# Optimization experiments

Hardware: AMD Instinct MI355X
Metric: run time of the kernel (lower is better)

## Reference

```python
import jax, jax.numpy as jnp
import numpy as np

B, SEQ, D, H, L, DFF, K = 2, 2048, 256, 8, 2, 1024, 3
DK = D // H
EPS = 1e-5
DROP_CONNECT = 0.5  # eval mode: weight * (1 - rate)


def _make_pe():
    pos = np.arange(SEQ)[:, None].astype(np.float32)
    div = np.exp(np.arange(0, D, 2).astype(np.float32) * (-np.log(10000.0) / D))
    pe = np.zeros((SEQ, D), np.float32)
    pe[:, 0::2] = np.sin(pos * div)
    pe[:, 1::2] = np.cos(pos * div)
    return jnp.asarray(pe)


def setup_inputs() -> dict:
    key = jax.random.key(0)
    ks = jax.random.split(key, 16)
    s = 0.02
    d = {
        'x': jax.random.normal(ks[0], (B, SEQ, 1), jnp.float32),
        'conv_w': jax.random.normal(ks[1], (D, 1, K), jnp.float32) * s,
        'conv_b': jnp.zeros((D,), jnp.float32),
        'bn_g': jnp.ones((D,), jnp.float32),
        'bn_b': jnp.zeros((D,), jnp.float32),
        'pe': _make_pe(),
        'qW': jax.random.normal(ks[2], (L, D, D), jnp.float32) * s,
        'qb': jnp.zeros((L, D), jnp.float32),
        'kW': jax.random.normal(ks[3], (L, D, D), jnp.float32) * s,
        'kb': jnp.zeros((L, D), jnp.float32),
        'vW': jax.random.normal(ks[4], (L, D, D), jnp.float32) * s,
        'vb': jnp.zeros((L, D), jnp.float32),
        'oW': jax.random.normal(ks[5], (L, D, D), jnp.float32) * s,
        'ob': jnp.zeros((L, D), jnp.float32),
        'scale': jnp.ones((L,), jnp.float32),
        'td': jnp.ones((L, H), jnp.float32),
        'ln1g': jnp.ones((L, D), jnp.float32),
        'ln1b': jnp.zeros((L, D), jnp.float32),
        'f1W': jax.random.normal(ks[6], (L, DFF, D), jnp.float32) * s,
        'f1b': jnp.zeros((L, DFF), jnp.float32),
        'f2W': jax.random.normal(ks[7], (L, D, DFF), jnp.float32) * s,
        'f2b': jnp.zeros((L, D), jnp.float32),
        'ln2g': jnp.ones((L, D), jnp.float32),
        'ln2b': jnp.zeros((L, D), jnp.float32),
        'outW': jax.random.normal(ks[8], (1, D), jnp.float32) * s,
        'outb': jnp.zeros((1,), jnp.float32),
    }
    return d


def _layernorm(z, g, b):
    m = z.mean(-1, keepdims=True)
    v = ((z - m) ** 2).mean(-1, keepdims=True)
    return (z - m) / jnp.sqrt(v + EPS) * g + b


def reference(x, conv_w, conv_b, bn_g, bn_b, pe, qW, qb, kW, kb, vW, vb, oW, ob,
              scale, td, ln1g, ln1b, f1W, f1b, f2W, f2b, ln2g, ln2b, outW, outb):
    # CNN frontend: [B,S,1] -> [B,1,S] -> conv -> BN(eval) -> relu -> [B,S,D]
    h = jnp.transpose(x, (0, 2, 1))
    h = jax.lax.conv_general_dilated(h, conv_w, (1,), 'SAME',
                                     dimension_numbers=('NCH', 'OIH', 'NCH'))
    h = h + conv_b[None, :, None]
    # BatchNorm eval with running_mean=0, running_var=1
    h = h / jnp.sqrt(1.0 + EPS) * bn_g[None, :, None] + bn_b[None, :, None]
    h = jax.nn.relu(h)
    h = jnp.transpose(h, (0, 2, 1)) + pe[None]

    inv_sqrt_dk = 1.0 / np.sqrt(DK).astype(np.float32)
    key_pos = jnp.arange(SEQ, dtype=h.dtype)  # decay depends on key index only

    for l in range(L):
        q = (h @ qW[l].T + qb[l]).reshape(B, SEQ, H, DK).transpose(0, 2, 1, 3)
        k = (h @ kW[l].T + kb[l]).reshape(B, SEQ, H, DK).transpose(0, 2, 1, 3)
        v = (h @ vW[l].T + vb[l]).reshape(B, SEQ, H, DK).transpose(0, 2, 1, 3)
        scores = jnp.einsum('bhqd,bhkd->bhqk', q, k) * (inv_sqrt_dk * scale[l])
        decay = jnp.exp(-td[l][:, None, None] * key_pos[None, None, :])  # [H,1,S]
        scores = scores * decay[None]
        attn = jax.nn.softmax(scores, axis=-1) * jax.nn.sigmoid(scores)
        ctx = jnp.einsum('bhqk,bhkd->bhqd', attn, v)
        ctx = ctx.transpose(0, 2, 1, 3).reshape(B, SEQ, D)
        h = _layernorm(h + (ctx @ oW[l].T + ob[l]), ln1g[l], ln1b[l])
        ff = jax.nn.relu(h @ f1W[l].T + f1b[l]) @ f2W[l].T + f2b[l]
        h = _layernorm(h + ff, ln2g[l], ln2b[l])

    last = h[:, -1, :]
    # DropConnectLinear in eval: weight * (1 - drop_connect_rate)
    return last @ (outW * (1.0 - DROP_CONNECT)).T + outb
```

## Files before the change

kernel.cpp:

```cpp
#include <hip/hip_runtime.h>
#include <math.h>

#define B_    2
#define SEQ_  2048
#define D_    256
#define H_    8
#define DK_   32
#define L_    2
#define DFF_  1024

#define TD_CUT 44.0f

typedef short  bf16x8 __attribute__((ext_vector_type(8)));
typedef float  f32x4  __attribute__((ext_vector_type(4)));

__device__ __forceinline__ int compute_kcut(float tdv) {
    int kcut = SEQ_;
    if (tdv > 1e-9f) {
        float kc = TD_CUT / tdv;
        kcut = (kc >= (float)SEQ_) ? SEQ_ : ((int)kc + 1);
    }
    int kcr = (kcut + 31) & ~31;
    if (kcr > SEQ_) kcr = SEQ_;
    return kcr;
}

__device__ __forceinline__ unsigned short f2bf(float f) {
    unsigned int u = __float_as_uint(f);
    unsigned int r = u + 0x7FFFu + ((u >> 16) & 1u);
    return (unsigned short)(r >> 16);
}
__device__ __forceinline__ float bf2f(unsigned short u) {
    return __uint_as_float(((unsigned int)u) << 16);
}

__device__ __forceinline__ void gload_lds16(const unsigned short* g, unsigned short* l) {
    __builtin_amdgcn_global_load_lds(
        (const __attribute__((address_space(1))) unsigned int*)(const unsigned int*)g,
        (__attribute__((address_space(3))) unsigned int*)(unsigned int*)l,
        16, 0, 0);
}

__global__ __launch_bounds__(256) void prep_kernel(
    const float* __restrict__ x, const float* __restrict__ w,
    const float* __restrict__ cb, const float* __restrict__ bg,
    const float* __restrict__ bb, const float* __restrict__ pe,
    float* __restrict__ h, unsigned short* __restrict__ hbf,
    const float* __restrict__ p0, const float* __restrict__ p1,
    const float* __restrict__ p2, const float* __restrict__ p3,
    const float* __restrict__ p4, const float* __restrict__ p5,
    unsigned short* __restrict__ q0, unsigned short* __restrict__ q1,
    unsigned short* __restrict__ q2, unsigned short* __restrict__ q3,
    unsigned short* __restrict__ q4, unsigned short* __restrict__ q5,
    float* __restrict__ vtail)
{
    int bid = blockIdx.x;
    if (bid < 4) vtail[bid * 256 + threadIdx.x] = 0.f;
    if (bid < 768) {
        int t = bid * 256 + threadIdx.x;
        const float* src; unsigned short* dst; int base;
        if (t < 65536) {
            int a = t >> 14;
            src = a == 0 ? p0 : a == 1 ? p1 : a == 2 ? p2 : p3;
            dst = a == 0 ? q0 : a == 1 ? q1 : a == 2 ? q2 : q3;
            base = (t & 16383) * 8;
        } else {
            int u = t - 65536;
            int a = u >> 16;
            src = a ? p5 : p4;
            dst = a ? q5 : q4;
            base = (u & 65535) * 8;
        }
        float4 v0 = *(const float4*)(src + base);
        float4 v1 = *(const float4*)(src + base + 4);
        bf16x8 o;
        o[0] = (short)f2bf(v0.x); o[1] = (short)f2bf(v0.y);
        o[2] = (short)f2bf(v0.z); o[3] = (short)f2bf(v0.w);
        o[4] = (short)f2bf(v1.x); o[5] = (short)f2bf(v1.y);
        o[6] = (short)f2bf(v1.z); o[7] = (short)f2bf(v1.w);
        *(bf16x8*)(dst + base) = o;
        return;
    }
    int idx = (bid - 768) * 256 + threadIdx.x;
    int d = idx & 255;
    int s = (idx >> 8) & 2047;
    int b = idx >> 19;

    const float* xp = x + b * SEQ_;
    float xm1 = (s > 0)        ? xp[s - 1] : 0.f;
    float x0  = xp[s];
    float xp1 = (s < SEQ_ - 1) ? xp[s + 1] : 0.f;

    float acc = xm1 * w[d * 3 + 0] + x0 * w[d * 3 + 1] + xp1 * w[d * 3 + 2];
    acc += cb[d];
    acc = acc * rsqrtf(1.f + 1e-5f) * bg[d] + bb[d];
    acc = fmaxf(acc, 0.f);
    float v = acc + pe[s * D_ + d];
    h[idx] = v;
    hbf[idx] = f2bf(v);
}

__global__ __launch_bounds__(256) void gemm_qkv(
    const unsigned short* __restrict__ A,
    const unsigned short* __restrict__ W0, const unsigned short* __restrict__ W1,
    const unsigned short* __restrict__ W2,
    const float* __restrict__ b0, const float* __restrict__ b1,
    const float* __restrict__ b2,
    unsigned short* __restrict__ O0, unsigned short* __restrict__ O1,
    unsigned short* __restrict__ O2,
    const float* __restrict__ td_l, float* __restrict__ vtail_l,
    int M, int N, int K)
{
    int z = blockIdx.z;
    const unsigned short* W = (z == 0) ? W0 : (z == 1) ? W1 : W2;
    const float* bias = (z == 0) ? b0 : (z == 1) ? b1 : b2;
    unsigned short* C = (z == 0) ? O0 : (z == 1) ? O1 : O2;

    __shared__ unsigned short As[64 * 32];
    __shared__ unsigned short Bs[64 * 32];
    __shared__ float vsc[4][2][16];

    int tid  = threadIdx.x;
    int wave = tid >> 6, lane = tid & 63;
    int wm = (wave & 1) * 32, wn = (wave >> 1) * 32;
    int bm = blockIdx.y * 64, bn = blockIdx.x * 64;

    int sr  = tid >> 2;
    int scb = (tid & 3) ^ ((sr >> 1) & 3);
    const unsigned short* aG = A + (size_t)(bm + sr) * K + scb * 8;
    const unsigned short* wG = W + (size_t)(bn + sr) * K + scb * 8;
    unsigned short* aL = &As[tid * 8];
    unsigned short* bL = &Bs[tid * 8];

    int fr = lane & 15;
    int kb = lane >> 4;
    int cb = (kb ^ ((fr >> 1) & 3)) * 8;
    int oA0 = (wm + fr) * 32 + cb;
    int oA1 = (wm + 16 + fr) * 32 + cb;
    int oB0 = (wn + fr) * 32 + cb;
    int oB1 = (wn + 16 + fr) * 32 + cb;

    f32x4 acc[2][2];
#pragma unroll
    for (int i = 0; i < 2; ++i)
#pragma unroll
        for (int j = 0; j < 2; ++j) acc[i][j] = (f32x4){0.f, 0.f, 0.f, 0.f};

    for (int k0 = 0; k0 < K; k0 += 32) {
        __syncthreads();
        gload_lds16(aG + k0, aL);
        gload_lds16(wG + k0, bL);
        __syncthreads();

        bf16x8 a0f = *(const bf16x8*)&As[oA0];
        bf16x8 a1f = *(const bf16x8*)&As[oA1];
        bf16x8 b0f = *(const bf16x8*)&Bs[oB0];
        bf16x8 b1f = *(const bf16x8*)&Bs[oB1];

        acc[0][0] = __builtin_amdgcn_mfma_f32_16x16x32_bf16(a0f, b0f, acc[0][0], 0, 0, 0);
        acc[0][1] = __builtin_amdgcn_mfma_f32_16x16x32_bf16(a0f, b1f, acc[0][1], 0, 0, 0);
        acc[1][0] = __builtin_amdgcn_mfma_f32_16x16x32_bf16(a1f, b0f, acc[1][0], 0, 0, 0);
        acc[1][1] = __builtin_amdgcn_mfma_f32_16x16x32_bf16(a1f, b1f, acc[1][1], 0, 0, 0);
    }

    int crow = (lane >> 4) * 4;
    int ccol = lane & 15;
    float psum[2] = {0.f, 0.f};
    int kc[2];
    kc[0] = compute_kcut(td_l[(bn + wn) >> 5]);
    kc[1] = compute_kcut(td_l[(bn + wn + 16) >> 5]);

#pragma unroll
    for (int j = 0; j < 2; ++j) {
        float bj = bias[bn + wn + j * 16 + ccol];
#pragma unroll
        for (int i = 0; i < 2; ++i) {
#pragma unroll
            for (int r = 0; r < 4; ++r) {
                float v = acc[i][j][r] + bj;
                unsigned short ubf = f2bf(v);
                C[(size_t)(bm + wm + i * 16 + crow + r) * N + bn + wn + j * 16 + ccol] = ubf;
                if (z == 2) {
                    int srow = (bm + wm + i * 16 + crow + r) & 2047;
                    if (srow >= kc[j]) psum[j] += bf2f(ubf);
                }
            }
        }
    }

    if (z == 2) {
#pragma unroll
        for (int j = 0; j < 2; ++j) {
            psum[j] += __shfl_xor(psum[j], 16);
            psum[j] += __shfl_xor(psum[j], 32);
        }
        if (lane < 16) { vsc[wave][0][lane] = psum[0]; vsc[wave][1][lane] = psum[1]; }
        __syncthreads();
        if (tid < 64) {
            int wh = tid >> 5, jj = (tid >> 4) & 1, cc = tid & 15;
            float s = vsc[2 * wh][jj][cc] + vsc[2 * wh + 1][jj][cc];
            int b = blockIdx.y >> 5;
            atomicAdd(&vtail_l[b * 256 + bn + wh * 32 + jj * 16 + cc], s);
        }
    }
}

__global__ __launch_bounds__(128) void attn_kernel(
    const unsigned short* __restrict__ q, const unsigned short* __restrict__ k,
    const unsigned short* __restrict__ v, const float* __restrict__ vtail_l,
    unsigned short* __restrict__ ctxbf,
    const float* __restrict__ scale_p, const float* __restrict__ td_l)
{
    int b = blockIdx.z, hh = blockIdx.y;
    int tid = threadIdx.x;
    int row = tid >> 2;
    int sp  = tid & 3;
    int qrow = blockIdx.x * 32 + row;

    float sc  = 0.17677669529663687f * scale_p[0];
    float tdv = td_l[hh];
    int kcr = compute_kcut(tdv);
    int ntiles = kcr >> 5;

    __shared__ float kt[32][36];
    __shared__ float vt[32][36];
    __shared__ float Os[4][32][36];
    __shared__ float ms[4][32], ls[4][32];
    __shared__ float vts[32];

    if (tid < 32) vts[tid] = vtail_l[b * 256 + hh * 32 + tid];

    const unsigned short* qptr = q + ((size_t)(b * SEQ_ + qrow)) * D_ + hh * DK_;
    float qreg[32];
#pragma unroll
    for (int j = 0; j < 4; ++j) {
        uint4 u = ((const uint4*)qptr)[j];
        qreg[j*8+0] = __uint_as_float(u.x << 16); qreg[j*8+1] = __uint_as_float(u.x & 0xFFFF0000u);
        qreg[j*8+2] = __uint_as_float(u.y << 16); qreg[j*8+3] = __uint_as_float(u.y & 0xFFFF0000u);
        qreg[j*8+4] = __uint_as_float(u.z << 16); qreg[j*8+5] = __uint_as_float(u.z & 0xFFFF0000u);
        qreg[j*8+6] = __uint_as_float(u.w << 16); qreg[j*8+7] = __uint_as_float(u.w & 0xFFFF0000u);
    }
    float O[32];
#pragma unroll
    for (int d = 0; d < 32; ++d) O[d] = 0.f;
    float mrun = -1e30f, lrun = 0.f;

    for (int t = 0; t < ntiles; ++t) {
        int k0 = t * 32;
        __syncthreads();
        {
            int r = tid >> 2, c8 = (tid & 3) * 8;
            size_t goff = ((size_t)(b * SEQ_ + k0 + r)) * D_ + hh * DK_ + c8;
            uint4 uk = *(const uint4*)(k + goff);
            uint4 uv = *(const uint4*)(v + goff);
            *(float4*)&kt[r][c8]     = make_float4(__uint_as_float(uk.x << 16), __uint_as_float(uk.x & 0xFFFF0000u),
                                                   __uint_as_float(uk.y << 16), __uint_as_float(uk.y & 0xFFFF0000u));
            *(float4*)&kt[r][c8 + 4] = make_float4(__uint_as_float(uk.z << 16), __uint_as_float(uk.z & 0xFFFF0000u),
                                                   __uint_as_float(uk.w << 16), __uint_as_float(uk.w & 0xFFFF0000u));
            *(float4*)&vt[r][c8]     = make_float4(__uint_as_float(uv.x << 16), __uint_as_float(uv.x & 0xFFFF0000u),
                                                   __uint_as_float(uv.y << 16), __uint_as_float(uv.y & 0xFFFF0000u));
            *(float4*)&vt[r][c8 + 4] = make_float4(__uint_as_float(uv.z << 16), __uint_as_float(uv.z & 0xFFFF0000u),
                                                   __uint_as_float(uv.w << 16), __uint_as_float(uv.w & 0xFFFF0000u));
        }
        __syncthreads();

        float sb[8];
        float tmax = -1e30f;
#pragma unroll
        for (int kk = 0; kk < 8; ++kk) {
            int kl = sp * 8 + kk;
            float acc = 0.f;
#pragma unroll
            for (int d4 = 0; d4 < 8; ++d4) {
                float4 kv = *(const float4*)&kt[kl][d4 * 4];
                acc += qreg[d4 * 4 + 0] * kv.x + qreg[d4 * 4 + 1] * kv.y
                     + qreg[d4 * 4 + 2] * kv.z + qreg[d4 * 4 + 3] * kv.w;
            }
            float dec = __expf(-tdv * (float)(k0 + kl));
            float sv = acc * sc * dec;
            sb[kk] = sv;
            tmax = fmaxf(tmax, sv);
        }
        float mnew = fmaxf(mrun, tmax);
        float alpha = __expf(mrun - mnew);
        lrun *= alpha;
#pragma unroll
        for (int d = 0; d < 32; ++d) O[d] *= alpha;
#pragma unroll
        for (int kk = 0; kk < 8; ++kk) {
            int kl = sp * 8 + kk;
            float sv = sb[kk];
            float e = __expf(sv - mnew);
            float sg = 1.f / (1.f + __expf(-sv));
            float p = e * sg;
            lrun += e;
#pragma unroll
            for (int d4 = 0; d4 < 8; ++d4) {
                float4 vv = *(const float4*)&vt[kl][d4 * 4];
                O[d4 * 4 + 0] += p * vv.x; O[d4 * 4 + 1] += p * vv.y;
                O[d4 * 4 + 2] += p * vv.z; O[d4 * 4 + 3] += p * vv.w;
            }
        }
        mrun = mnew;
    }

#pragma unroll
    for (int d4 = 0; d4 < 8; ++d4)
        *(float4*)&Os[sp][row][d4 * 4] =
            make_float4(O[d4*4+0], O[d4*4+1], O[d4*4+2], O[d4*4+3]);
    ms[sp][row] = mrun;
    ls[sp][row] = lrun;
    __syncthreads();

    {
        int g = sp;
        float m0 = fmaxf(fmaxf(ms[0][row], ms[1][row]), fmaxf(ms[2][row], ms[3][row]));
        float mt = (kcr < SEQ_) ? fmaxf(m0, 0.f) : m0;
        float w0 = __expf(ms[0][row] - mt), w1 = __expf(ms[1][row] - mt);
        float w2 = __expf(ms[2][row] - mt), w3 = __expf(ms[3][row] - mt);
        float Lt = ls[0][row]*w0 + ls[1][row]*w1 + ls[2][row]*w2 + ls[3][row]*w3;
        float ew = 0.f;
        if (kcr < SEQ_) {
            ew = __expf(-mt);
            Lt += (float)(SEQ_ - kcr) * ew;
        }
        float invL = 1.f / Lt;
        unsigned int packed[4];
#pragma unroll
        for (int dd = 0; dd < 8; dd += 2) {
            int d0 = g * 8 + dd, d1 = d0 + 1;
            float n0 = Os[0][row][d0]*w0 + Os[1][row][d0]*w1 + Os[2][row][d0]*w2 + Os[3][row][d0]*w3;
            float n1 = Os[0][row][d1]*w0 + Os[1][row][d1]*w1 + Os[2][row][d1]*w2 + Os[3][row][d1]*w3;
            if (kcr < SEQ_) {
                n0 += 0.5f * ew * vts[d0];
                n1 += 0.5f * ew * vts[d1];
            }
            packed[dd >> 1] = (unsigned)f2bf(n0 * invL) | ((unsigned)f2bf(n1 * invL) << 16);
        }
        unsigned short* obf = ctxbf + ((size_t)(b * SEQ_ + qrow)) * D_ + hh * DK_ + g * 8;
        *(uint4*)obf = make_uint4(packed[0], packed[1], packed[2], packed[3]);
    }
}

__global__ __launch_bounds__(256) void oproj_ln1(
    const unsigned short* __restrict__ ctx, const unsigned short* __restrict__ wo,
    const float* __restrict__ ob, const float* __restrict__ resid,
    const float* __restrict__ g1, const float* __restrict__ bt1,
    float* __restrict__ h1out, unsigned short* __restrict__ h1bf)
{
    __shared__ unsigned short As[16 * 32];
    __shared__ unsigned short Bs[256 * 32];
    __shared__ float lsum[4][16], lsq[4][16], mean_s[16], inv_s[16];

    int tid = threadIdx.x;
    int wave = tid >> 6, lane = tid & 63;
    int bm = blockIdx.x * 16;
    int fr = lane & 15, kb = lane >> 4;
    int q = kb, cl = fr;
    int swz = (fr >> 1) & 3;

    const unsigned short* gpB[4];
    unsigned short* lpB[4];
#pragma unroll
    for (int i = 0; i < 4; ++i) {
        int sB = i * 256 + tid;
        int r = sB >> 2, ck = (sB & 3) ^ ((r >> 1) & 3);
        gpB[i] = wo + (size_t)r * 256 + ck * 8;
        lpB[i] = &Bs[sB * 8];
    }
    const unsigned short* gpA = nullptr;
    unsigned short* lpA = nullptr;
    if (tid < 64) {
        int r = tid >> 2, ck = (tid & 3) ^ ((r >> 1) & 3);
        gpA = ctx + (size_t)(bm + r) * 256 + ck * 8;
        lpA = &As[tid * 8];
    }

    int oA = fr * 32 + ((kb ^ swz) * 8);
    int oB[4];
#pragma unroll
    for (int t = 0; t < 4; ++t) {
        int n = wave * 64 + t * 16 + fr;
        oB[t] = n * 32 + ((kb ^ swz) * 8);
    }

    f32x4 acc[4];
#pragma unroll
    for (int j = 0; j < 4; ++j) acc[j] = (f32x4){0.f, 0.f, 0.f, 0.f};

    for (int k0 = 0; k0 < 256; k0 += 32) {
        __syncthreads();
#pragma unroll
        for (int i = 0; i < 4; ++i) gload_lds16(gpB[i] + k0, lpB[i]);
        if (tid < 64) gload_lds16(gpA + k0, lpA);
        __syncthreads();

        bf16x8 af = *(const bf16x8*)&As[oA];
#pragma unroll
        for (int j = 0; j < 4; ++j)
            acc[j] = __builtin_amdgcn_mfma_f32_16x16x32_bf16(
                af, *(const bf16x8*)&Bs[oB[j]], acc[j], 0, 0, 0);
    }

    float zsum[4] = {0.f, 0.f, 0.f, 0.f}, zsq[4] = {0.f, 0.f, 0.f, 0.f};
    float zv[4][4];
#pragma unroll
    for (int ct = 0; ct < 4; ++ct) {
        int col = wave * 64 + ct * 16 + cl;
        float bj = ob[col];
#pragma unroll
        for (int r = 0; r < 4; ++r) {
            int row = bm + q * 4 + r;
            float z = acc[ct][r] + bj + resid[(size_t)row * 256 + col];
            zv[ct][r] = z;
            zsum[r] += z;
            zsq[r]  += z * z;
        }
    }
#pragma unroll
    for (int r = 0; r < 4; ++r) {
#pragma unroll
        for (int off = 1; off < 16; off <<= 1) {
            zsum[r] += __shfl_xor(zsum[r], off);
            zsq[r]  += __shfl_xor(zsq[r], off);
        }
    }
    if (cl == 0) {
#pragma unroll
        for (int r = 0; r < 4; ++r) {
            lsum[wave][q * 4 + r] = zsum[r];
            lsq[wave][q * 4 + r]  = zsq[r];
        }
    }
    __syncthreads();
    if (tid < 16) {
        float s  = lsum[0][tid] + lsum[1][tid] + lsum[2][tid] + lsum[3][tid];
        float sq = lsq[0][tid] + lsq[1][tid] + lsq[2][tid] + lsq[3][tid];
        float mean = s * (1.f / 256.f);
        float var  = sq * (1.f / 256.f) - mean * mean;
        mean_s[tid] = mean;
        inv_s[tid]  = rsqrtf(var + 1e-5f);
    }
    __syncthreads();

#pragma unroll
    for (int ct = 0; ct < 4; ++ct) {
        int col = wave * 64 + ct * 16 + cl;
        float gc = g1[col], bc = bt1[col];
#pragma unroll
        for (int r = 0; r < 4; ++r) {
            int lr = q * 4 + r;
            float o = (zv[ct][r] - mean_s[lr]) * inv_s[lr] * gc + bc;
            size_t off = (size_t)(bm + lr) * 256 + col;
            h1out[off] = o;
            h1bf[off]  = f2bf(o);
        }
    }
}

__global__ __launch_bounds__(256) void ffn_fused(
    const unsigned short* __restrict__ h1bf, const unsigned short* __restrict__ w1,
    const float* __restrict__ f1b, const unsigned short* __restrict__ w2,
    float* __restrict__ part)
{
    __shared__ unsigned short As[32 * 32];
    __shared__ unsigned short Bs[256 * 32];
    __shared__ unsigned short ffs[32 * 264];

    int tid = threadIdx.x;
    int wave = tid >> 6, lane = tid & 63;
    int c = blockIdx.x;
    int bm = blockIdx.y * 32;
    int fr = lane & 15, kb = lane >> 4;
    int q = kb, cl = fr;
    int swz = (fr >> 1) & 3;

    const unsigned short* gA = nullptr;
    unsigned short* lA = nullptr;
    if (tid < 128) {
        int ar = tid >> 2, ack = (tid & 3) ^ ((ar >> 1) & 3);
        gA = h1bf + (size_t)(bm + ar) * 256 + ack * 8;
        lA = &As[tid * 8];
    }

    int oA1[2], oB[4];
#pragma unroll
    for (int t = 0; t < 2; ++t) {
        int m = t * 16 + fr;
        oA1[t] = m * 32 + ((kb ^ ((m >> 1) & 3)) * 8);
    }
#pragma unroll
    for (int t = 0; t < 4; ++t) {
        int n = wave * 64 + t * 16 + fr;
        oB[t] = n * 32 + ((kb ^ ((n >> 1) & 3)) * 8);
    }

    f32x4 a1[2][4];
#pragma unroll
    for (int i = 0; i < 2; ++i)
#pragma unroll
        for (int j = 0; j < 4; ++j) a1[i][j] = (f32x4){0.f, 0.f, 0.f, 0.f};

    for (int ks = 0; ks < 8; ++ks) {
        __syncthreads();
        if (tid < 128) gload_lds16(gA + ks * 32, lA);
#pragma unroll
        for (int i = 0; i < 4; ++i) {
            int sB = i * 256 + tid;
            int r = sB >> 2, ck = (sB & 3) ^ ((r >> 1) & 3);
            gload_lds16(w1 + (size_t)(c * 256 + r) * 256 + ks * 32 + ck * 8, &Bs[sB * 8]);
        }
        __syncthreads();

        bf16x8 af[2], bfv[4];
#pragma unroll
        for (int t = 0; t < 2; ++t) af[t] = *(const bf16x8*)&As[oA1[t]];
#pragma unroll
        for (int t = 0; t < 4; ++t) bfv[t] = *(const bf16x8*)&Bs[oB[t]];
#pragma unroll
        for (int i = 0; i < 2; ++i)
#pragma unroll
            for (int j = 0; j < 4; ++j)
                a1[i][j] = __builtin_amdgcn_mfma_f32_16x16x32_bf16(af[i], bfv[j], a1[i][j], 0, 0, 0);
    }

#pragma unroll
    for (int ct = 0; ct < 4; ++ct) {
        int col = wave * 64 + ct * 16 + cl;
        float bj = f1b[c * 256 + col];
#pragma unroll
        for (int rt = 0; rt < 2; ++rt)
#pragma unroll
            for (int r = 0; r < 4; ++r) {
                float v = fmaxf(a1[rt][ct][r] + bj, 0.f);
                ffs[(rt * 16 + q * 4 + r) * 264 + col] = f2bf(v);
            }
    }

    f32x4 a2[2][4];
#pragma unroll
    for (int i = 0; i < 2; ++i)
#pragma unroll
        for (int j = 0; j < 4; ++j) a2[i][j] = (f32x4){0.f, 0.f, 0.f, 0.f};

    for (int ks = 0; ks < 8; ++ks) {
        __syncthreads();
#pragma unroll
        for (int i = 0; i < 4; ++i) {
            int sB = i * 256 + tid;
            int r = sB >> 2, ck = (sB & 3) ^ ((r >> 1) & 3);
            gload_lds16(w2 + (size_t)r * 1024 + c * 256 + ks * 32 + ck * 8, &Bs[sB * 8]);
        }
        __syncthreads();

        bf16x8 af[2], bfv[4];
#pragma unroll
        for (int t = 0; t < 2; ++t)
            af[t] = *(const bf16x8*)&ffs[(t * 16 + fr) * 264 + ks * 32 + kb * 8];
#pragma unroll
        for (int t = 0; t < 4; ++t) bfv[t] = *(const bf16x8*)&Bs[oB[t]];
#pragma unroll
        for (int i = 0; i < 2; ++i)
#pragma unroll
            for (int j = 0; j < 4; ++j)
                a2[i][j] = __builtin_amdgcn_mfma_f32_16x16x32_bf16(af[i], bfv[j], a2[i][j], 0, 0, 0);
    }

#pragma unroll
    for (int ct = 0; ct < 4; ++ct) {
        int col = wave * 64 + ct * 16 + cl;
#pragma unroll
        for (int rt = 0; rt < 2; ++rt)
#pragma unroll
            for (int r = 0; r < 4; ++r)
                part[((size_t)c * 4096 + bm + rt * 16 + q * 4 + r) * 256 + col] = a2[rt][ct][r];
    }
}

__global__ __launch_bounds__(256) void merge_ln2(
    const float* __restrict__ h1, const float* __restrict__ part,
    const float* __restrict__ f2b, const float* __restrict__ g2,
    const float* __restrict__ bt2,
    float* __restrict__ hout, unsigned short* __restrict__ hbf,
    const float* __restrict__ outW, const float* __restrict__ outb,
    float* __restrict__ out, int doFinal)
{
    int row = blockIdx.x * 4 + (threadIdx.x >> 6);
    int lane = threadIdx.x & 63;
    int d = lane * 4;

    float4 z = *(const float4*)(h1 + (size_t)row * 256 + d);
    float4 b4 = *(const float4*)(f2b + d);
    z.x += b4.x; z.y += b4.y; z.z += b4.z; z.w += b4.w;
#pragma unroll
    for (int c = 0; c < 4; ++c) {
        float4 p = *(const float4*)(part + ((size_t)c * 4096 + row) * 256 + d);
        z.x += p.x; z.y += p.y; z.z += p.z; z.w += p.w;
    }

    float s = z.x + z.y + z.z + z.w;
    float ss = z.x * z.x + z.y * z.y + z.z * z.z + z.w * z.w;
#pragma unroll
    for (int off = 1; off < 64; off <<= 1) {
        s += __shfl_xor(s, off);
        ss += __shfl_xor(ss, off);
    }
    float mean = s * (1.f / 256.f);
    float var = ss * (1.f / 256.f) - mean * mean;
    float inv = rsqrtf(var + 1e-5f);

    float4 g4 = *(const float4*)(g2 + d);
    float4 t4 = *(const float4*)(bt2 + d);
    float4 o;
    o.x = (z.x - mean) * inv * g4.x + t4.x;
    o.y = (z.y - mean) * inv * g4.y + t4.y;
    o.z = (z.z - mean) * inv * g4.z + t4.z;
    o.w = (z.w - mean) * inv * g4.w + t4.w;
    *(float4*)(hout + (size_t)row * 256 + d) = o;
    unsigned int u01 = (unsigned)f2bf(o.x) | ((unsigned)f2bf(o.y) << 16);
    unsigned int u23 = (unsigned)f2bf(o.z) | ((unsigned)f2bf(o.w) << 16);
    *(uint2*)&hbf[(size_t)row * 256 + d] = make_uint2(u01, u23);

    if (doFinal && (row == 2047 || row == 4095)) {
        float4 w4 = *(const float4*)(outW + d);
        float s2 = o.x * w4.x + o.y * w4.y + o.z * w4.z + o.w * w4.w;
#pragma unroll
        for (int off = 1; off < 64; off <<= 1) s2 += __shfl_xor(s2, off);
        if (lane == 0) out[row >> 11] = s2 * 0.5f + outb[0];
    }
}

extern "C" void kernel_launch(void* const* d_in, const int* in_sizes, int n_in,
                              void* d_out, int out_size, void* d_ws, size_t ws_size,
                              hipStream_t stream)
{
    (void)in_sizes; (void)n_in; (void)out_size; (void)ws_size;
    const float* x      = (const float*)d_in[0];
    const float* conv_w = (const float*)d_in[1];
    const float* conv_b = (const float*)d_in[2];
    const float* bn_g   = (const float*)d_in[3];
    const float* bn_b   = (const float*)d_in[4];
    const float* pe     = (const float*)d_in[5];
    const float* qW     = (const float*)d_in[6];
    const float* qb     = (const float*)d_in[7];
    const float* kW     = (const float*)d_in[8];
    const float* kb     = (const float*)d_in[9];
    const float* vW     = (const float*)d_in[10];
    const float* vb     = (const float*)d_in[11];
    const float* oW     = (const float*)d_in[12];
    const float* ob     = (const float*)d_in[13];
    const float* scale  = (const float*)d_in[14];
    const float* td     = (const float*)d_in[15];
    const float* ln1g   = (const float*)d_in[16];
    const float* ln1b   = (const float*)d_in[17];
    const float* f1W    = (const float*)d_in[18];
    const float* f1b    = (const float*)d_in[19];
    const float* f2W    = (const float*)d_in[20];
    const float* f2b    = (const float*)d_in[21];
    const float* ln2g   = (const float*)d_in[22];
    const float* ln2b   = (const float*)d_in[23];
    const float* outW   = (const float*)d_in[24];
    const float* outb   = (const float*)d_in[25];
    float* out = (float*)d_out;

    float* ws = (float*)d_ws;
    const size_t MT = (size_t)B_ * SEQ_ * D_;
    float* h     = ws;
    float* h1    = ws + MT;
    float* part  = ws + 2 * MT;
    float* vtail = ws + 6 * MT;
    unsigned short* bfb = (unsigned short*)(ws + 6 * MT + 1024);
    unsigned short* h_bf   = bfb;
    unsigned short* ctx_bf = bfb + MT;
    unsigned short* q_bf   = bfb + 2 * MT;
    unsigned short* k_bf   = bfb + 3 * MT;
    unsigned short* v_bf   = bfb + 4 * MT;
    unsigned short* h1_bf  = bfb + 5 * MT;
    unsigned short* wq_bf  = bfb + 6 * MT;
    unsigned short* wk_bf  = wq_bf + MT / 8;
    unsigned short* wv_bf  = wk_bf + MT / 8;
    unsigned short* wo_bf  = wv_bf + MT / 8;
    unsigned short* wf1_bf = wo_bf + MT / 8;
    unsigned short* wf2_bf = wf1_bf + MT / 2;

    const int Mrows = B_ * SEQ_;

    prep_kernel<<<768 + (B_ * SEQ_ * D_) / 256, 256, 0, stream>>>(
        x, conv_w, conv_b, bn_g, bn_b, pe, h, h_bf,
        qW, kW, vW, oW, f1W, f2W,
        wq_bf, wk_bf, wv_bf, wo_bf, wf1_bf, wf2_bf, vtail);

    for (int l = 0; l < L_; ++l) {
        const unsigned short* wq_l  = wq_bf  + (size_t)l * D_ * D_;
        const unsigned short* wk_l  = wk_bf  + (size_t)l * D_ * D_;
        const unsigned short* wv_l  = wv_bf  + (size_t)l * D_ * D_;
        const unsigned short* wo_l  = wo_bf  + (size_t)l * D_ * D_;
        const unsigned short* wf1_l = wf1_bf + (size_t)l * DFF_ * D_;
        const unsigned short* wf2_l = wf2_bf + (size_t)l * DFF_ * D_;
        float* vtail_l = vtail + l * B_ * 256;

        gemm_qkv<<<dim3(D_ / 64, Mrows / 64, 3), 256, 0, stream>>>(
            h_bf, wq_l, wk_l, wv_l, qb + l * D_, kb + l * D_, vb + l * D_,
            q_bf, k_bf, v_bf, td + l * H_, vtail_l, Mrows, D_, D_);

        attn_kernel<<<dim3(SEQ_ / 32, H_, B_), 128, 0, stream>>>(
            q_bf, k_bf, v_bf, vtail_l, ctx_bf, scale + l, td + l * H_);

        oproj_ln1<<<Mrows / 16, 256, 0, stream>>>(
            ctx_bf, wo_l, ob + l * D_, h,
            ln1g + l * D_, ln1b + l * D_, h1, h1_bf);

        ffn_fused<<<dim3(4, Mrows / 32), 256, 0, stream>>>(
            h1_bf, wf1_l, f1b + l * DFF_, wf2_l, part);

        merge_ln2<<<Mrows / 4, 256, 0, stream>>>(
            h1, part, f2b + l * D_, ln2g + l * D_, ln2b + l * D_,
            h, h_bf, outW, outb, out, (l == L_ - 1) ? 1 : 0);
    }
}
```

Before: 204.9 us.

## Double GEMM K-tile to 64 with XOR swizzle and halve oproj row tile

Widens the K tile from 32 to 64 in the QKV, o-proj and FFN GEMMs and switches to an 8-way XOR swizzle, so each main loop needs half as many barrier pairs and the MFMAs see twice the work per sync. The o-proj+LN1 kernel now handles 8 rows per block instead of 16, with zero padding in LDS for the unused MFMA rows, which doubles the grid for more parallelism. In exchange, LDS use per block grows (the o-proj B tile goes from 16 KB to 32 KB, and FFN uses more too), which may lower occupancy. Half of the o-proj MFMA rows are now wasted work, and the wo weights are reloaded by twice as many blocks.

```diff
diff --git a/kernel.cpp b/kernel.cpp
--- a/kernel.cpp
+++ b/kernel.cpp
@@ -116,8 +116,8 @@
     const float* bias = (z == 0) ? b0 : (z == 1) ? b1 : b2;
     unsigned short* C = (z == 0) ? O0 : (z == 1) ? O1 : O2;
 
-    __shared__ unsigned short As[64 * 32];
-    __shared__ unsigned short Bs[64 * 32];
+    __shared__ unsigned short As[64 * 64];
+    __shared__ unsigned short Bs[64 * 64];
     __shared__ float vsc[4][2][16];
 
     int tid  = threadIdx.x;
@@ -125,20 +125,22 @@
     int wm = (wave & 1) * 32, wn = (wave >> 1) * 32;
     int bm = blockIdx.y * 64, bn = blockIdx.x * 64;
 
-    int sr  = tid >> 2;
-    int scb = (tid & 3) ^ ((sr >> 1) & 3);
-    const unsigned short* aG = A + (size_t)(bm + sr) * K + scb * 8;
-    const unsigned short* wG = W + (size_t)(bn + sr) * K + scb * 8;
-    unsigned short* aL = &As[tid * 8];
-    unsigned short* bL = &Bs[tid * 8];
+    const unsigned short* aG[2]; unsigned short* aL[2];
+    const unsigned short* wG[2]; unsigned short* bL[2];
+#pragma unroll
+    for (int i = 0; i < 2; ++i) {
+        int s = i * 256 + tid;
+        int r = s >> 3, cb8 = s & 7;
+        int gofs = ((cb8 ^ (r & 7)) * 8);
+        aG[i] = A + (size_t)(bm + r) * K + gofs;
+        aL[i] = &As[s * 8];
+        wG[i] = W + (size_t)(bn + r) * K + gofs;
+        bL[i] = &Bs[s * 8];
+    }
 
     int fr = lane & 15;
     int kb = lane >> 4;
-    int cb = (kb ^ ((fr >> 1) & 3)) * 8;
-    int oA0 = (wm + fr) * 32 + cb;
-    int oA1 = (wm + 16 + fr) * 32 + cb;
-    int oB0 = (wn + fr) * 32 + cb;
-    int oB1 = (wn + 16 + fr) * 32 + cb;
+    int swz = fr & 7;
 
     f32x4 acc[2][2];
 #pragma unroll
@@ -146,29 +148,36 @@
 #pragma unroll
         for (int j = 0; j < 2; ++j) acc[i][j] = (f32x4){0.f, 0.f, 0.f, 0.f};
 
-    for (int k0 = 0; k0 < K; k0 += 32) {
-        __syncthreads();
-        gload_lds16(aG + k0, aL);
-        gload_lds16(wG + k0, bL);
-        __syncthreads();
-
-        bf16x8 a0f = *(const bf16x8*)&As[oA0];
-        bf16x8 a1f = *(const bf16x8*)&As[oA1];
-        bf16x8 b0f = *(const bf16x8*)&Bs[oB0];
-        bf16x8 b1f = *(const bf16x8*)&Bs[oB1];
-
-        acc[0][0] = __builtin_amdgcn_mfma_f32_16x16x32_bf16(a0f, b0f, acc[0][0], 0, 0, 0);
-        acc[0][1] = __builtin_amdgcn_mfma_f32_16x16x32_bf16(a0f, b1f, acc[0][1], 0, 0, 0);
-        acc[1][0] = __builtin_amdgcn_mfma_f32_16x16x32_bf16(a1f, b0f, acc[1][0], 0, 0, 0);
-        acc[1][1] = __builtin_amdgcn_mfma_f32_16x16x32_bf16(a1f, b1f, acc[1][1], 0, 0, 0);
+    for (int k0 = 0; k0 < K; k0 += 64) {
+        __syncthreads();
+#pragma unroll
+        for (int i = 0; i < 2; ++i) {
+            gload_lds16(aG[i] + k0, aL[i]);
+            gload_lds16(wG[i] + k0, bL[i]);
+        }
+        __syncthreads();
+
+#pragma unroll
+        for (int kc = 0; kc < 2; ++kc) {
+            int blk = ((kc * 4 + kb) ^ swz) * 8;
+            bf16x8 a0f = *(const bf16x8*)&As[(wm + fr) * 64 + blk];
+            bf16x8 a1f = *(const bf16x8*)&As[(wm + 16 + fr) * 64 + blk];
+            bf16x8 b0f = *(const bf16x8*)&Bs[(wn + fr) * 64 + blk];
+            bf16x8 b1f = *(const bf16x8*)&Bs[(wn + 16 + fr) * 64 + blk];
+
+            acc[0][0] = __builtin_amdgcn_mfma_f32_16x16x32_bf16(a0f, b0f, acc[0][0], 0, 0, 0);
+            acc[0][1] = __builtin_amdgcn_mfma_f32_16x16x32_bf16(a0f, b1f, acc[0][1], 0, 0, 0);
+            acc[1][0] = __builtin_amdgcn_mfma_f32_16x16x32_bf16(a1f, b0f, acc[1][0], 0, 0, 0);
+            acc[1][1] = __builtin_amdgcn_mfma_f32_16x16x32_bf16(a1f, b1f, acc[1][1], 0, 0, 0);
+        }
     }
 
     int crow = (lane >> 4) * 4;
     int ccol = lane & 15;
     float psum[2] = {0.f, 0.f};
-    int kc[2];
-    kc[0] = compute_kcut(td_l[(bn + wn) >> 5]);
-    kc[1] = compute_kcut(td_l[(bn + wn + 16) >> 5]);
+    int kc2[2];
+    kc2[0] = compute_kcut(td_l[(bn + wn) >> 5]);
+    kc2[1] = compute_kcut(td_l[(bn + wn + 16) >> 5]);
 
 #pragma unroll
     for (int j = 0; j < 2; ++j) {
@@ -182,7 +191,7 @@
                 C[(size_t)(bm + wm + i * 16 + crow + r) * N + bn + wn + j * 16 + ccol] = ubf;
                 if (z == 2) {
                     int srow = (bm + wm + i * 16 + crow + r) & 2047;
-                    if (srow >= kc[j]) psum[j] += bf2f(ubf);
+                    if (srow >= kc2[j]) psum[j] += bf2f(ubf);
                 }
             }
         }
@@ -348,58 +357,53 @@
     const float* __restrict__ g1, const float* __restrict__ bt1,
     float* __restrict__ h1out, unsigned short* __restrict__ h1bf)
 {
-    __shared__ unsigned short As[16 * 32];
-    __shared__ unsigned short Bs[256 * 32];
+    __shared__ unsigned short As[16 * 64];
+    __shared__ unsigned short Bs[256 * 64];
     __shared__ float lsum[4][16], lsq[4][16], mean_s[16], inv_s[16];
 
     int tid = threadIdx.x;
     int wave = tid >> 6, lane = tid & 63;
-    int bm = blockIdx.x * 16;
+    int bm = blockIdx.x * 8;
     int fr = lane & 15, kb = lane >> 4;
     int q = kb, cl = fr;
-    int swz = (fr >> 1) & 3;
-
-    const unsigned short* gpB[4];
-    unsigned short* lpB[4];
-#pragma unroll
-    for (int i = 0; i < 4; ++i) {
-        int sB = i * 256 + tid;
-        int r = sB >> 2, ck = (sB & 3) ^ ((r >> 1) & 3);
-        gpB[i] = wo + (size_t)r * 256 + ck * 8;
-        lpB[i] = &Bs[sB * 8];
-    }
-    const unsigned short* gpA = nullptr;
-    unsigned short* lpA = nullptr;
+    int swz = fr & 7;
+
+    ((unsigned int*)As)[256 + tid] = 0u;
+
+    const unsigned short* gA = nullptr;
+    unsigned short* lA = nullptr;
     if (tid < 64) {
-        int r = tid >> 2, ck = (tid & 3) ^ ((r >> 1) & 3);
-        gpA = ctx + (size_t)(bm + r) * 256 + ck * 8;
-        lpA = &As[tid * 8];
-    }
-
-    int oA = fr * 32 + ((kb ^ swz) * 8);
-    int oB[4];
-#pragma unroll
-    for (int t = 0; t < 4; ++t) {
-        int n = wave * 64 + t * 16 + fr;
-        oB[t] = n * 32 + ((kb ^ swz) * 8);
+        int r = tid >> 3, cb8 = tid & 7;
+        gA = ctx + (size_t)(bm + r) * 256 + ((cb8 ^ (r & 7)) * 8);
+        lA = &As[tid * 8];
     }
 
     f32x4 acc[4];
 #pragma unroll
     for (int j = 0; j < 4; ++j) acc[j] = (f32x4){0.f, 0.f, 0.f, 0.f};
 
-    for (int k0 = 0; k0 < 256; k0 += 32) {
-        __syncthreads();
-#pragma unroll
-        for (int i = 0; i < 4; ++i) gload_lds16(gpB[i] + k0, lpB[i]);
-        if (tid < 64) gload_lds16(gpA + k0, lpA);
-        __syncthreads();
-
-        bf16x8 af = *(const bf16x8*)&As[oA];
-#pragma unroll
-        for (int j = 0; j < 4; ++j)
-            acc[j] = __builtin_amdgcn_mfma_f32_16x16x32_bf16(
-                af, *(const bf16x8*)&Bs[oB[j]], acc[j], 0, 0, 0);
+    for (int k0 = 0; k0 < 256; k0 += 64) {
+        __syncthreads();
+        if (tid < 64) gload_lds16(gA + k0, lA);
+#pragma unroll
+        for (int i = 0; i < 8; ++i) {
+            int s = i * 256 + tid;
+            int r = s >> 3, cb8 = s & 7;
+            gload_lds16(wo + (size_t)r * 256 + k0 + ((cb8 ^ (r & 7)) * 8), &Bs[s * 8]);
+        }
+        __syncthreads();
+
+#pragma unroll
+        for (int kc = 0; kc < 2; ++kc) {
+            int blk = ((kc * 4 + kb) ^ swz) * 8;
+            bf16x8 af = *(const bf16x8*)&As[fr * 64 + blk];
+#pragma unroll
+            for (int t = 0; t < 4; ++t) {
+                int n = wave * 64 + t * 16 + fr;
+                bf16x8 bfv = *(const bf16x8*)&Bs[n * 64 + blk];
+                acc[t] = __builtin_amdgcn_mfma_f32_16x16x32_bf16(af, bfv, acc[t], 0, 0, 0);
+            }
+        }
     }
 
     float zsum[4] = {0.f, 0.f, 0.f, 0.f}, zsq[4] = {0.f, 0.f, 0.f, 0.f};
@@ -410,8 +414,9 @@
         float bj = ob[col];
 #pragma unroll
         for (int r = 0; r < 4; ++r) {
-            int row = bm + q * 4 + r;
-            float z = acc[ct][r] + bj + resid[(size_t)row * 256 + col];
+            int lr = q * 4 + r;
+            float z = 0.f;
+            if (lr < 8) z = acc[ct][r] + bj + resid[(size_t)(bm + lr) * 256 + col];
             zv[ct][r] = z;
             zsum[r] += z;
             zsq[r]  += z * z;
@@ -450,10 +455,12 @@
 #pragma unroll
         for (int r = 0; r < 4; ++r) {
             int lr = q * 4 + r;
-            float o = (zv[ct][r] - mean_s[lr]) * inv_s[lr] * gc + bc;
-            size_t off = (size_t)(bm + lr) * 256 + col;
-            h1out[off] = o;
-            h1bf[off]  = f2bf(o);
+            if (lr < 8) {
+                float o = (zv[ct][r] - mean_s[lr]) * inv_s[lr] * gc + bc;
+                size_t off = (size_t)(bm + lr) * 256 + col;
+                h1out[off] = o;
+                h1bf[off]  = f2bf(o);
+            }
         }
     }
 }
@@ -463,8 +470,8 @@
     const float* __restrict__ f1b, const unsigned short* __restrict__ w2,
     float* __restrict__ part)
 {
-    __shared__ unsigned short As[32 * 32];
-    __shared__ unsigned short Bs[256 * 32];
+    __shared__ unsigned short As[32 * 64];
+    __shared__ unsigned short Bs[256 * 64];
     __shared__ unsigned short ffs[32 * 264];
 
     int tid = threadIdx.x;
@@ -473,27 +480,11 @@
     int bm = blockIdx.y * 32;
     int fr = lane & 15, kb = lane >> 4;
     int q = kb, cl = fr;
-    int swz = (fr >> 1) & 3;
-
-    const unsigned short* gA = nullptr;
-    unsigned short* lA = nullptr;
-    if (tid < 128) {
-        int ar = tid >> 2, ack = (tid & 3) ^ ((ar >> 1) & 3);
-        gA = h1bf + (size_t)(bm + ar) * 256 + ack * 8;
-        lA = &As[tid * 8];
-    }
-
-    int oA1[2], oB[4];
-#pragma unroll
-    for (int t = 0; t < 2; ++t) {
-        int m = t * 16 + fr;
-        oA1[t] = m * 32 + ((kb ^ ((m >> 1) & 3)) * 8);
-    }
-#pragma unroll
-    for (int t = 0; t < 4; ++t) {
-        int n = wave * 64 + t * 16 + fr;
-        oB[t] = n * 32 + ((kb ^ ((n >> 1) & 3)) * 8);
-    }
+    int swz = fr & 7;
+
+    int ar = tid >> 3, acb = tid & 7;
+    const unsigned short* gA = h1bf + (size_t)(bm + ar) * 256 + ((acb ^ (ar & 7)) * 8);
+    unsigned short* lA = &As[tid * 8];
 
     f32x4 a1[2][4];
 #pragma unroll
@@ -501,27 +492,34 @@
 #pragma unroll
         for (int j = 0; j < 4; ++j) a1[i][j] = (f32x4){0.f, 0.f, 0.f, 0.f};
 
-    for (int ks = 0; ks < 8; ++ks) {
-        __syncthreads();
-        if (tid < 128) gload_lds16(gA + ks * 32, lA);
-#pragma unroll
-        for (int i = 0; i < 4; ++i) {
-            int sB = i * 256 + tid;
-            int r = sB >> 2, ck = (sB & 3) ^ ((r >> 1) & 3);
-            gload_lds16(w1 + (size_t)(c * 256 + r) * 256 + ks * 32 + ck * 8, &Bs[sB * 8]);
-        }
-        __syncthreads();
-
-        bf16x8 af[2], bfv[4];
-#pragma unroll
-        for (int t = 0; t < 2; ++t) af[t] = *(const bf16x8*)&As[oA1[t]];
-#pragma unroll
-        for (int t = 0; t < 4; ++t) bfv[t] = *(const bf16x8*)&Bs[oB[t]];
-#pragma unroll
-        for (int i = 0; i < 2; ++i)
-#pragma unroll
-            for (int j = 0; j < 4; ++j)
-                a1[i][j] = __builtin_amdgcn_mfma_f32_16x16x32_bf16(af[i], bfv[j], a1[i][j], 0, 0, 0);
+    for (int k0 = 0; k0 < 256; k0 += 64) {
+        __syncthreads();
+        gload_lds16(gA + k0, lA);
+#pragma unroll
+        for (int i = 0; i < 8; ++i) {
+            int s = i * 256 + tid;
+            int r = s >> 3, cb8 = s & 7;
+            gload_lds16(w1 + (size_t)(c * 256 + r) * 256 + k0 + ((cb8 ^ (r & 7)) * 8), &Bs[s * 8]);
+        }
+        __syncthreads();
+
+#pragma unroll
+        for (int kc = 0; kc < 2; ++kc) {
+            int blk = ((kc * 4 + kb) ^ swz) * 8;
+            bf16x8 af[2], bfv[4];
+#pragma unroll
+            for (int t = 0; t < 2; ++t) af[t] = *(const bf16x8*)&As[(t * 16 + fr) * 64 + blk];
+#pragma unroll
+            for (int t = 0; t < 4; ++t) {
+                int n = wave * 64 + t * 16 + fr;
+                bfv[t] = *(const bf16x8*)&Bs[n * 64 + blk];
+            }
+#pragma unroll
+            for (int i = 0; i < 2; ++i)
+#pragma unroll
+                for (int j = 0; j < 4; ++j)
+                    a1[i][j] = __builtin_amdgcn_mfma_f32_16x16x32_bf16(af[i], bfv[j], a1[i][j], 0, 0, 0);
+        }
     }
 
 #pragma unroll
@@ -543,27 +541,34 @@
 #pragma unroll
         for (int j = 0; j < 4; ++j) a2[i][j] = (f32x4){0.f, 0.f, 0.f, 0.f};
 
-    for (int ks = 0; ks < 8; ++ks) {
-        __syncthreads();
-#pragma unroll
-        for (int i = 0; i < 4; ++i) {
-            int sB = i * 256 + tid;
-            int r = sB >> 2, ck = (sB & 3) ^ ((r >> 1) & 3);
-            gload_lds16(w2 + (size_t)r * 1024 + c * 256 + ks * 32 + ck * 8, &Bs[sB * 8]);
-        }
-        __syncthreads();
-
-        bf16x8 af[2], bfv[4];
-#pragma unroll
-        for (int t = 0; t < 2; ++t)
-            af[t] = *(const bf16x8*)&ffs[(t * 16 + fr) * 264 + ks * 32 + kb * 8];
-#pragma unroll
-        for (int t = 0; t < 4; ++t) bfv[t] = *(const bf16x8*)&Bs[oB[t]];
-#pragma unroll
-        for (int i = 0; i < 2; ++i)
-#pragma unroll
-            for (int j = 0; j < 4; ++j)
-                a2[i][j] = __builtin_amdgcn_mfma_f32_16x16x32_bf16(af[i], bfv[j], a2[i][j], 0, 0, 0);
+    for (int k0 = 0; k0 < 256; k0 += 64) {
+        __syncthreads();
+#pragma unroll
+        for (int i = 0; i < 8; ++i) {
+            int s = i * 256 + tid;
+            int r = s >> 3, cb8 = s & 7;
+            gload_lds16(w2 + (size_t)r * 1024 + c * 256 + k0 + ((cb8 ^ (r & 7)) * 8), &Bs[s * 8]);
+        }
+        __syncthreads();
+
+#pragma unroll
+        for (int kc = 0; kc < 2; ++kc) {
+            int blk = ((kc * 4 + kb) ^ swz) * 8;
+            bf16x8 af[2], bfv[4];
+#pragma unroll
+            for (int t = 0; t < 2; ++t)
+                af[t] = *(const bf16x8*)&ffs[(t * 16 + fr) * 264 + k0 + kc * 32 + kb * 8];
+#pragma unroll
+            for (int t = 0; t < 4; ++t) {
+                int n = wave * 64 + t * 16 + fr;
+                bfv[t] = *(const bf16x8*)&Bs[n * 64 + blk];
+            }
+#pragma unroll
+            for (int i = 0; i < 2; ++i)
+#pragma unroll
+                for (int j = 0; j < 4; ++j)
+                    a2[i][j] = __builtin_amdgcn_mfma_f32_16x16x32_bf16(af[i], bfv[j], a2[i][j], 0, 0, 0);
+        }
     }
 
 #pragma unroll
@@ -706,7 +711,7 @@
         attn_kernel<<<dim3(SEQ_ / 32, H_, B_), 128, 0, stream>>>(
             q_bf, k_bf, v_bf, vtail_l, ctx_bf, scale + l, td + l * H_);
 
-        oproj_ln1<<<Mrows / 16, 256, 0, stream>>>(
+        oproj_ln1<<<Mrows / 8, 256, 0, stream>>>(
             ctx_bf, wo_l, ob + l * D_, h,
             ln1g + l * D_, ln1b + l * D_, h1, h1_bf);
 
```

Result: no change. 206.7 us (+0.9%).
